# Optimization experiments

Measured on AMD Instinct MI355X. Metric: run time of the kernel, lower is better.

## Reference

```python
import jax, jax.numpy as jnp
import numpy as np

B, IN, H = 1024, 2048, 2048
W_BIT = A_BIT = I_BIT = R_BIT = 8


def fake_quant(x, bits):
    # brevitas CommonQuant: signed, narrow-range, const scale 1.0 ->
    # int scale s = 1/(2^(b-1)-1); q = clip(round(x/s), -n, n); dq = q*s.
    n = 2.0 ** (bits - 1) - 1.0
    q = jnp.clip(x * n, -n, n)
    q = q + jax.lax.stop_gradient(jnp.round(q) - q)  # STE round
    return q / n


def setup_inputs() -> dict:
    key = jax.random.key(0)
    ks = jax.random.split(key, 7)
    std = 1.0 / np.sqrt(H)  # reset_parameters: uniform(-std, std)
    return {
        "x": jax.random.normal(ks[0], (B, IN), jnp.float32),
        "hx": jax.random.normal(ks[1], (B, H), jnp.float32),
        "cx": jax.random.normal(ks[2], (B, H), jnp.float32),
        "w_x2h": jax.random.uniform(ks[3], (4 * H, IN), jnp.float32, -std, std),
        "b_x2h": jax.random.uniform(ks[4], (4 * H,), jnp.float32, -std, std),
        "w_h2h": jax.random.uniform(ks[5], (4 * H, H), jnp.float32, -std, std),
        "b_h2h": jax.random.uniform(ks[6], (4 * H,), jnp.float32, -std, std),
    }


def reference(x, hx, cx, w_x2h, b_x2h, w_h2h, b_h2h):
    x_q = fake_quant(x, I_BIT)                      # input_quant
    wx_q = fake_quant(w_x2h, W_BIT)                 # CommonWeightQuant
    wh_q = fake_quant(w_h2h, W_BIT)
    gates = (jnp.einsum('bi,gi->bg', x_q, wx_q) + b_x2h
             + jnp.einsum('bh,gh->bg', hx, wh_q) + b_h2h)  # [B, 4H]
    f, i, g, o = jnp.split(gates, 4, axis=1)        # forget, input, cell, out
    f = fake_quant(jax.nn.sigmoid(f), A_BIT)
    i = fake_quant(jax.nn.sigmoid(i), A_BIT)
    g = fake_quant(jnp.tanh(g), A_BIT)
    o = fake_quant(jax.nn.sigmoid(o), A_BIT)
    c_new = f * cx + i * g
    h_new = o * fake_quant(jnp.tanh(c_new), A_BIT)
    c_out = fake_quant(c_new, R_BIT)                # recurrent_quant
    return (h_new, c_out)
```

## Files before the change

kernel.cpp:

```cpp
#include <hip/hip_runtime.h>
#include <stdint.h>
#include <math.h>

typedef __attribute__((ext_vector_type(4))) int i32x4;
typedef __attribute__((ext_vector_type(4))) float f32x4;

#define GLD16(gp, lp)                                                     \
  __builtin_amdgcn_global_load_lds(                                       \
      (__attribute__((address_space(1))) void*)(gp),                      \
      (__attribute__((address_space(3))) void*)(lp), 16, 0, 0)

__global__ void __launch_bounds__(256) k_prep_w(const float* __restrict__ wx,
                                                const float* __restrict__ wh,
                                                signed char* __restrict__ Wq) {
  int i = blockIdx.x * 256 + threadIdx.x;
  int e = i << 2;
  int g = e >> 12;
  int c = e & 4095;
  const float* src = (c < 2048) ? (wx + g * 2048 + c) : (wh + g * 2048 + (c - 2048));
  float4 v = *(const float4*)src;
  char4 o;
  o.x = (signed char)(int)rint(fmin(fmax((double)v.x * 127.0, -127.0), 127.0));
  o.y = (signed char)(int)rint(fmin(fmax((double)v.y * 127.0, -127.0), 127.0));
  o.z = (signed char)(int)rint(fmin(fmax((double)v.z * 127.0, -127.0), 127.0));
  o.w = (signed char)(int)rint(fmin(fmax((double)v.w * 127.0, -127.0), 127.0));
  *(char4*)(Wq + e) = o;
}

__global__ void __launch_bounds__(256) k_prep_a(const float* __restrict__ x,
                                                const float* __restrict__ hx,
                                                signed char* __restrict__ Aq) {
  int i = blockIdx.x * 256 + threadIdx.x;
  int e = i << 2;
  int b = e >> 11;
  int c = e & 2047;
  float4 xv = *(const float4*)(x + b * 2048 + c);
  float4 hv = *(const float4*)(hx + b * 2048 + c);
  float xa[4] = {xv.x, xv.y, xv.z, xv.w};
  float ha[4] = {hv.x, hv.y, hv.z, hv.w};
  char4 q4, s1, s2, s3, s4, s5;
  signed char* qp = (signed char*)&q4;
  signed char* p1 = (signed char*)&s1;
  signed char* p2 = (signed char*)&s2;
  signed char* p3 = (signed char*)&s3;
  signed char* p4 = (signed char*)&s4;
  signed char* p5 = (signed char*)&s5;
  #pragma unroll
  for (int j = 0; j < 4; ++j) {
    qp[j] = (signed char)(int)rint(fmin(fmax((double)xa[j] * 127.0, -127.0), 127.0));
    double r = (double)ha[j];
    double d1 = rint(r * 16.0);     r -= d1 * 0x1p-4;
    double d2 = rint(r * 0x1p11);   r -= d2 * 0x1p-11;
    double d3 = rint(r * 0x1p18);   r -= d3 * 0x1p-18;
    double d4 = rint(r * 0x1p25);   r -= d4 * 0x1p-25;
    double d5 = rint(r * 0x1p32);
    p1[j] = (signed char)(int)d1;
    p2[j] = (signed char)(int)d2;
    p3[j] = (signed char)(int)d3;
    p4[j] = (signed char)(int)d4;
    p5[j] = (signed char)(int)d5;
  }
  size_t base = (size_t)b * 12288;
  *(char4*)(Aq + base + 0 * 2048 + c) = s5;
  *(char4*)(Aq + base + 1 * 2048 + c) = s4;
  *(char4*)(Aq + base + 2 * 2048 + c) = s3;
  *(char4*)(Aq + base + 3 * 2048 + c) = s2;
  *(char4*)(Aq + base + 4 * 2048 + c) = s1;
  *(char4*)(Aq + base + 5 * 2048 + c) = q4;
}

__global__ void __launch_bounds__(256, 3) k_gemm_lstm(
    const signed char* __restrict__ Aq, const signed char* __restrict__ Wq,
    const float* __restrict__ bx, const float* __restrict__ bh,
    const float* __restrict__ cx, float* __restrict__ out) {
  __shared__ __align__(16) signed char smem[24576];
  signed char* As = smem;
  signed char* Bs = smem + 16384;

  const int t  = threadIdx.x;
  const int wv = t >> 6;
  const int ln = t & 63;
  const int wm = wv & 1;
  const int wn = wv >> 1;
  const int lr = ln & 15;
  const int q  = ln >> 4;

  const int j0 = blockIdx.x * 16;
  const int m0 = blockIdx.y * 128;

  int sA[4];
  #pragma unroll
  for (int is = 0; is < 4; ++is) {
    int s = is * 256 + t;
    int r = s >> 3;
    int c = s & 7;
    int cp = c ^ (r & 7);
    sA[is] = (m0 + r) * 12288 + cp * 16;
  }
  int sB[2];
  #pragma unroll
  for (int is = 0; is < 2; ++is) {
    int s = is * 256 + t;
    int r = s >> 3;
    int c = s & 7;
    int cp = c ^ (r & 7);
    int wrow = (r >> 4) * 2048 + j0 + (r & 15);
    sB[is] = wrow * 4096 + cp * 16;
  }

  int aoff[4], boff[2];
  const int swz = lr & 7;
  #pragma unroll
  for (int mf = 0; mf < 4; ++mf)
    aoff[mf] = (wm * 64 + mf * 16 + lr) * 128 + ((q ^ swz) * 16);
  #pragma unroll
  for (int nf = 0; nf < 2; ++nf)
    boff[nf] = (wn * 32 + nf * 16 + lr) * 128 + ((q ^ swz) * 16);

  i32x4 acc[4][2];
  f32x4 Hh[4][2], Hl[4][2];
  #pragma unroll
  for (int mf = 0; mf < 4; ++mf)
    #pragma unroll
    for (int nf = 0; nf < 2; ++nf)
      acc[mf][nf] = (i32x4){0, 0, 0, 0};

  #pragma unroll 1
  for (int ph = 0; ph < 6; ++ph) {
    const int kA = ph * 2048;
    const int kB = (ph < 5) ? 2048 : 0;
    #pragma unroll 1
    for (int it = 0; it < 16; ++it) {
      const int kk = it * 128;
      __syncthreads();
      #pragma unroll
      for (int is = 0; is < 4; ++is)
        GLD16(Aq + sA[is] + kA + kk, As + is * 4096 + wv * 1024);
      #pragma unroll
      for (int is = 0; is < 2; ++is)
        GLD16(Wq + sB[is] + kB + kk, Bs + is * 4096 + wv * 1024);
      asm volatile("s_waitcnt vmcnt(0)" ::: "memory");
      __syncthreads();
      #pragma unroll
      for (int s = 0; s < 2; ++s) {
        const int sx = s << 6;
        i32x4 af[4], bf[2];
        #pragma unroll
        for (int mf = 0; mf < 4; ++mf) af[mf] = *(const i32x4*)&As[aoff[mf] ^ sx];
        #pragma unroll
        for (int nf = 0; nf < 2; ++nf) bf[nf] = *(const i32x4*)&Bs[boff[nf] ^ sx];
        #pragma unroll
        for (int mf = 0; mf < 4; ++mf)
          #pragma unroll
          for (int nf = 0; nf < 2; ++nf)
            acc[mf][nf] = __builtin_amdgcn_mfma_i32_16x16x64_i8(
                af[mf], bf[nf], acc[mf][nf], 0, 0, 0);
      }
    }
    if (ph == 0) {
      #pragma unroll
      for (int mf = 0; mf < 4; ++mf)
        #pragma unroll
        for (int nf = 0; nf < 2; ++nf) {
          #pragma unroll
          for (int r = 0; r < 4; ++r) {
            Hh[mf][nf][r] = (float)acc[mf][nf][r];
            Hl[mf][nf][r] = 0.f;
          }
          acc[mf][nf] = (i32x4){0, 0, 0, 0};
        }
    } else if (ph < 5) {
      #pragma unroll
      for (int mf = 0; mf < 4; ++mf)
        #pragma unroll
        for (int nf = 0; nf < 2; ++nf) {
          #pragma unroll
          for (int r = 0; r < 4; ++r) {
            float tv = Hh[mf][nf][r] * 0x1p-7f;
            float S  = (float)acc[mf][nf][r];
            float sm = tv + S;
            float z  = sm - tv;
            float e  = (tv - (sm - z)) + (S - z);
            Hl[mf][nf][r] = Hl[mf][nf][r] * 0x1p-7f + e;
            Hh[mf][nf][r] = sm;
          }
          acc[mf][nf] = (i32x4){0, 0, 0, 0};
        }
    }
  }

  const double invsq = 1.0 / 16129.0;
  const double hsc   = 0x1p-4 / 127.0;

  float (*Lgo)[128][17] = (float(*)[128][17])smem;

  __syncthreads();
  if (wn == 1) {
    #pragma unroll
    for (int mf = 0; mf < 4; ++mf) {
      #pragma unroll
      for (int nf = 0; nf < 2; ++nf) {
        int gate = 2 + nf;
        int gcol = gate * 2048 + j0 + lr;
        double bsum = (double)bx[gcol] + (double)bh[gcol];
        #pragma unroll
        for (int r = 0; r < 4; ++r) {
          double Sx = (double)acc[mf][nf][r];
          double Hd = ((double)Hh[mf][nf][r] + (double)Hl[mf][nf][r]) * hsc;
          double pre = Sx * invsq + Hd + bsum;
          double av = (gate == 2) ? tanh(pre) : (1.0 / (1.0 + exp(-pre)));
          double qv = rint(fmin(fmax(av * 127.0, -127.0), 127.0));
          int m = wm * 64 + mf * 16 + q * 4 + r;
          Lgo[nf][m][lr] = (float)qv;
        }
      }
    }
  }
  __syncthreads();
  if (wn == 0) {
    #pragma unroll
    for (int mf = 0; mf < 4; ++mf) {
      int gcf = j0 + lr;
      int gci = 2048 + j0 + lr;
      double bf_ = (double)bx[gcf] + (double)bh[gcf];
      double bi_ = (double)bx[gci] + (double)bh[gci];
      #pragma unroll
      for (int r = 0; r < 4; ++r) {
        int m = wm * 64 + mf * 16 + q * 4 + r;
        double fpre = (double)acc[mf][0][r] * invsq +
                      ((double)Hh[mf][0][r] + (double)Hl[mf][0][r]) * hsc + bf_;
        double ipre = (double)acc[mf][1][r] * invsq +
                      ((double)Hh[mf][1][r] + (double)Hl[mf][1][r]) * hsc + bi_;
        double fs = 1.0 / (1.0 + exp(-fpre));
        double is = 1.0 / (1.0 + exp(-ipre));
        double fv = rint(fmin(fmax(fs * 127.0, -127.0), 127.0)) / 127.0;
        double iv = rint(fmin(fmax(is * 127.0, -127.0), 127.0)) / 127.0;
        double gv = (double)Lgo[0][m][lr] / 127.0;
        double ov = (double)Lgo[1][m][lr] / 127.0;
        int row = m0 + m;
        int col = j0 + lr;
        double cn = fv * (double)cx[row * 2048 + col] + iv * gv;
        double tq = rint(fmin(fmax(tanh(cn) * 127.0, -127.0), 127.0)) / 127.0;
        double hv = ov * tq;
        double cq = rint(fmin(fmax(cn * 127.0, -127.0), 127.0)) / 127.0;
        out[row * 2048 + col] = (float)hv;
        out[2097152 + row * 2048 + col] = (float)cq;
      }
    }
  }
}

extern "C" void kernel_launch(void* const* d_in, const int* in_sizes, int n_in,
                              void* d_out, int out_size, void* d_ws, size_t ws_size,
                              hipStream_t stream) {
  const float* x  = (const float*)d_in[0];
  const float* hx = (const float*)d_in[1];
  const float* cx = (const float*)d_in[2];
  const float* wx = (const float*)d_in[3];
  const float* bx = (const float*)d_in[4];
  const float* wh = (const float*)d_in[5];
  const float* bh = (const float*)d_in[6];
  float* out = (float*)d_out;

  signed char* Wq = (signed char*)d_ws;
  signed char* Aq = (signed char*)d_ws + 33554432;

  k_prep_w<<<dim3(32768), dim3(256), 0, stream>>>(wx, wh, Wq);
  k_prep_a<<<dim3(2048), dim3(256), 0, stream>>>(x, hx, Aq);
  k_gemm_lstm<<<dim3(128, 8), dim3(256), 0, stream>>>(Aq, Wq, bx, bh, cx, out);
}
```

Baseline: 387.5 us.

## Widen GEMM tile to 32 columns, deepen K step, use float prep quantization

The prep kernels now quantize in float rather than double, cutting double-precision work. The GEMM block tile grows from 128x16 to 128x32 output columns per gate, with a 256-byte K step per iteration and a 64 KB LDS footprint. Occupancy drops to one block per CU, and the grid halves to 64x8. The hidden-state residue accumulation changes from a float two-sum to a plain double accumulator, trading register pressure and FP64 adds for simpler code.

```diff
diff --git a/kernel.cpp b/kernel.cpp
--- a/kernel.cpp
+++ b/kernel.cpp
@@ -3,7 +3,6 @@
 #include <math.h>
 
 typedef __attribute__((ext_vector_type(4))) int i32x4;
-typedef __attribute__((ext_vector_type(4))) float f32x4;
 
 #define GLD16(gp, lp)                                                     \
   __builtin_amdgcn_global_load_lds(                                       \
@@ -20,10 +19,10 @@
   const float* src = (c < 2048) ? (wx + g * 2048 + c) : (wh + g * 2048 + (c - 2048));
   float4 v = *(const float4*)src;
   char4 o;
-  o.x = (signed char)(int)rint(fmin(fmax((double)v.x * 127.0, -127.0), 127.0));
-  o.y = (signed char)(int)rint(fmin(fmax((double)v.y * 127.0, -127.0), 127.0));
-  o.z = (signed char)(int)rint(fmin(fmax((double)v.z * 127.0, -127.0), 127.0));
-  o.w = (signed char)(int)rint(fmin(fmax((double)v.w * 127.0, -127.0), 127.0));
+  o.x = (signed char)(int)rintf(fminf(fmaxf(v.x * 127.0f, -127.0f), 127.0f));
+  o.y = (signed char)(int)rintf(fminf(fmaxf(v.y * 127.0f, -127.0f), 127.0f));
+  o.z = (signed char)(int)rintf(fminf(fmaxf(v.z * 127.0f, -127.0f), 127.0f));
+  o.w = (signed char)(int)rintf(fminf(fmaxf(v.w * 127.0f, -127.0f), 127.0f));
   *(char4*)(Wq + e) = o;
 }
 
@@ -47,13 +46,13 @@
   signed char* p5 = (signed char*)&s5;
   #pragma unroll
   for (int j = 0; j < 4; ++j) {
-    qp[j] = (signed char)(int)rint(fmin(fmax((double)xa[j] * 127.0, -127.0), 127.0));
-    double r = (double)ha[j];
-    double d1 = rint(r * 16.0);     r -= d1 * 0x1p-4;
-    double d2 = rint(r * 0x1p11);   r -= d2 * 0x1p-11;
-    double d3 = rint(r * 0x1p18);   r -= d3 * 0x1p-18;
-    double d4 = rint(r * 0x1p25);   r -= d4 * 0x1p-25;
-    double d5 = rint(r * 0x1p32);
+    qp[j] = (signed char)(int)rintf(fminf(fmaxf(xa[j] * 127.0f, -127.0f), 127.0f));
+    float r = ha[j];
+    float d1 = rintf(r * 0x1p4f);    r -= d1 * 0x1p-4f;
+    float d2 = rintf(r * 0x1p11f);   r -= d2 * 0x1p-11f;
+    float d3 = rintf(r * 0x1p18f);   r -= d3 * 0x1p-18f;
+    float d4 = rintf(r * 0x1p25f);   r -= d4 * 0x1p-25f;
+    float d5 = rintf(r * 0x1p32f);
     p1[j] = (signed char)(int)d1;
     p2[j] = (signed char)(int)d2;
     p3[j] = (signed char)(int)d3;
@@ -69,13 +68,13 @@
   *(char4*)(Aq + base + 5 * 2048 + c) = q4;
 }
 
-__global__ void __launch_bounds__(256, 3) k_gemm_lstm(
+__global__ void __launch_bounds__(256, 1) k_gemm_lstm(
     const signed char* __restrict__ Aq, const signed char* __restrict__ Wq,
     const float* __restrict__ bx, const float* __restrict__ bh,
     const float* __restrict__ cx, float* __restrict__ out) {
-  __shared__ __align__(16) signed char smem[24576];
+  __shared__ __align__(16) signed char smem[65536];
   signed char* As = smem;
-  signed char* Bs = smem + 16384;
+  signed char* Bs = smem + 32768;
 
   const int t  = threadIdx.x;
   const int wv = t >> 6;
@@ -85,44 +84,35 @@
   const int lr = ln & 15;
   const int q  = ln >> 4;
 
-  const int j0 = blockIdx.x * 16;
+  const int j0 = blockIdx.x * 32;
   const int m0 = blockIdx.y * 128;
 
-  int sA[4];
-  #pragma unroll
-  for (int is = 0; is < 4; ++is) {
-    int s = is * 256 + t;
-    int r = s >> 3;
-    int c = s & 7;
-    int cp = c ^ (r & 7);
-    sA[is] = (m0 + r) * 12288 + cp * 16;
-  }
-  int sB[2];
-  #pragma unroll
-  for (int is = 0; is < 2; ++is) {
-    int s = is * 256 + t;
-    int r = s >> 3;
-    int c = s & 7;
-    int cp = c ^ (r & 7);
-    int wrow = (r >> 4) * 2048 + j0 + (r & 15);
-    sB[is] = wrow * 4096 + cp * 16;
-  }
-
-  int aoff[4], boff[2];
-  const int swz = lr & 7;
-  #pragma unroll
-  for (int mf = 0; mf < 4; ++mf)
-    aoff[mf] = (wm * 64 + mf * 16 + lr) * 128 + ((q ^ swz) * 16);
-  #pragma unroll
-  for (int nf = 0; nf < 2; ++nf)
-    boff[nf] = (wn * 32 + nf * 16 + lr) * 128 + ((q ^ swz) * 16);
-
-  i32x4 acc[4][2];
-  f32x4 Hh[4][2], Hl[4][2];
+  int sA[8], sB[8];
+  #pragma unroll
+  for (int i = 0; i < 8; ++i) {
+    int s = i * 256 + t;
+    int r = s >> 4;
+    int p = s & 15;
+    int c = p ^ (r & 15);
+    sA[i] = (m0 + r) * 12288 + c * 16;
+    int gate = r >> 5;
+    int jj = r & 31;
+    sB[i] = (gate * 2048 + j0 + jj) * 4096 + c * 16;
+  }
+
+  int aoff[4], boff[4];
+  #pragma unroll
+  for (int f = 0; f < 4; ++f) {
+    aoff[f] = (wm * 64 + f * 16 + lr) * 256;
+    boff[f] = 32768 + (wn * 64 + f * 16 + lr) * 256;
+  }
+
+  i32x4 acc[4][4];
+  double Hd[4][4][4];
   #pragma unroll
   for (int mf = 0; mf < 4; ++mf)
     #pragma unroll
-    for (int nf = 0; nf < 2; ++nf)
+    for (int nf = 0; nf < 4; ++nf)
       acc[mf][nf] = (i32x4){0, 0, 0, 0};
 
   #pragma unroll 1
@@ -130,88 +120,70 @@
     const int kA = ph * 2048;
     const int kB = (ph < 5) ? 2048 : 0;
     #pragma unroll 1
-    for (int it = 0; it < 16; ++it) {
-      const int kk = it * 128;
+    for (int it = 0; it < 8; ++it) {
+      const int kk = it * 256;
       __syncthreads();
       #pragma unroll
-      for (int is = 0; is < 4; ++is)
-        GLD16(Aq + sA[is] + kA + kk, As + is * 4096 + wv * 1024);
-      #pragma unroll
-      for (int is = 0; is < 2; ++is)
-        GLD16(Wq + sB[is] + kB + kk, Bs + is * 4096 + wv * 1024);
+      for (int i = 0; i < 8; ++i)
+        GLD16(Aq + sA[i] + kA + kk, As + i * 4096 + wv * 1024);
+      #pragma unroll
+      for (int i = 0; i < 8; ++i)
+        GLD16(Wq + sB[i] + kB + kk, Bs + i * 4096 + wv * 1024);
       asm volatile("s_waitcnt vmcnt(0)" ::: "memory");
       __syncthreads();
       #pragma unroll
-      for (int s = 0; s < 2; ++s) {
-        const int sx = s << 6;
-        i32x4 af[4], bf[2];
-        #pragma unroll
-        for (int mf = 0; mf < 4; ++mf) af[mf] = *(const i32x4*)&As[aoff[mf] ^ sx];
-        #pragma unroll
-        for (int nf = 0; nf < 2; ++nf) bf[nf] = *(const i32x4*)&Bs[boff[nf] ^ sx];
+      for (int kst = 0; kst < 4; ++kst) {
+        const int poff = ((kst * 4 + q) ^ lr) * 16;
+        i32x4 af[4], bf[4];
+        #pragma unroll
+        for (int mf = 0; mf < 4; ++mf) af[mf] = *(const i32x4*)&As[aoff[mf] + poff];
+        #pragma unroll
+        for (int nf = 0; nf < 4; ++nf) bf[nf] = *(const i32x4*)&smem[boff[nf] + poff];
         #pragma unroll
         for (int mf = 0; mf < 4; ++mf)
           #pragma unroll
-          for (int nf = 0; nf < 2; ++nf)
+          for (int nf = 0; nf < 4; ++nf)
             acc[mf][nf] = __builtin_amdgcn_mfma_i32_16x16x64_i8(
                 af[mf], bf[nf], acc[mf][nf], 0, 0, 0);
       }
     }
-    if (ph == 0) {
+    if (ph < 5) {
       #pragma unroll
       for (int mf = 0; mf < 4; ++mf)
         #pragma unroll
-        for (int nf = 0; nf < 2; ++nf) {
+        for (int nf = 0; nf < 4; ++nf) {
           #pragma unroll
           for (int r = 0; r < 4; ++r) {
-            Hh[mf][nf][r] = (float)acc[mf][nf][r];
-            Hl[mf][nf][r] = 0.f;
+            double S = (double)acc[mf][nf][r];
+            Hd[mf][nf][r] = (ph == 0) ? S : Hd[mf][nf][r] * 0x1p-7 + S;
           }
           acc[mf][nf] = (i32x4){0, 0, 0, 0};
         }
-    } else if (ph < 5) {
-      #pragma unroll
-      for (int mf = 0; mf < 4; ++mf)
-        #pragma unroll
-        for (int nf = 0; nf < 2; ++nf) {
-          #pragma unroll
-          for (int r = 0; r < 4; ++r) {
-            float tv = Hh[mf][nf][r] * 0x1p-7f;
-            float S  = (float)acc[mf][nf][r];
-            float sm = tv + S;
-            float z  = sm - tv;
-            float e  = (tv - (sm - z)) + (S - z);
-            Hl[mf][nf][r] = Hl[mf][nf][r] * 0x1p-7f + e;
-            Hh[mf][nf][r] = sm;
-          }
-          acc[mf][nf] = (i32x4){0, 0, 0, 0};
-        }
     }
   }
 
   const double invsq = 1.0 / 16129.0;
   const double hsc   = 0x1p-4 / 127.0;
 
-  float (*Lgo)[128][17] = (float(*)[128][17])smem;
+  float (*Lgo)[128][33] = (float(*)[128][33])smem;
 
   __syncthreads();
   if (wn == 1) {
     #pragma unroll
     for (int mf = 0; mf < 4; ++mf) {
       #pragma unroll
-      for (int nf = 0; nf < 2; ++nf) {
-        int gate = 2 + nf;
-        int gcol = gate * 2048 + j0 + lr;
+      for (int nf = 0; nf < 4; ++nf) {
+        int gate = 2 + (nf >> 1);
+        int jj = (nf & 1) * 16 + lr;
+        int gcol = gate * 2048 + j0 + jj;
         double bsum = (double)bx[gcol] + (double)bh[gcol];
         #pragma unroll
         for (int r = 0; r < 4; ++r) {
-          double Sx = (double)acc[mf][nf][r];
-          double Hd = ((double)Hh[mf][nf][r] + (double)Hl[mf][nf][r]) * hsc;
-          double pre = Sx * invsq + Hd + bsum;
+          double pre = (double)acc[mf][nf][r] * invsq + Hd[mf][nf][r] * hsc + bsum;
           double av = (gate == 2) ? tanh(pre) : (1.0 / (1.0 + exp(-pre)));
           double qv = rint(fmin(fmax(av * 127.0, -127.0), 127.0));
           int m = wm * 64 + mf * 16 + q * 4 + r;
-          Lgo[nf][m][lr] = (float)qv;
+          Lgo[gate - 2][m][jj] = (float)qv;
         }
       }
     }
@@ -220,31 +192,31 @@
   if (wn == 0) {
     #pragma unroll
     for (int mf = 0; mf < 4; ++mf) {
-      int gcf = j0 + lr;
-      int gci = 2048 + j0 + lr;
-      double bf_ = (double)bx[gcf] + (double)bh[gcf];
-      double bi_ = (double)bx[gci] + (double)bh[gci];
-      #pragma unroll
-      for (int r = 0; r < 4; ++r) {
-        int m = wm * 64 + mf * 16 + q * 4 + r;
-        double fpre = (double)acc[mf][0][r] * invsq +
-                      ((double)Hh[mf][0][r] + (double)Hl[mf][0][r]) * hsc + bf_;
-        double ipre = (double)acc[mf][1][r] * invsq +
-                      ((double)Hh[mf][1][r] + (double)Hl[mf][1][r]) * hsc + bi_;
-        double fs = 1.0 / (1.0 + exp(-fpre));
-        double is = 1.0 / (1.0 + exp(-ipre));
-        double fv = rint(fmin(fmax(fs * 127.0, -127.0), 127.0)) / 127.0;
-        double iv = rint(fmin(fmax(is * 127.0, -127.0), 127.0)) / 127.0;
-        double gv = (double)Lgo[0][m][lr] / 127.0;
-        double ov = (double)Lgo[1][m][lr] / 127.0;
-        int row = m0 + m;
-        int col = j0 + lr;
-        double cn = fv * (double)cx[row * 2048 + col] + iv * gv;
-        double tq = rint(fmin(fmax(tanh(cn) * 127.0, -127.0), 127.0)) / 127.0;
-        double hv = ov * tq;
-        double cq = rint(fmin(fmax(cn * 127.0, -127.0), 127.0)) / 127.0;
-        out[row * 2048 + col] = (float)hv;
-        out[2097152 + row * 2048 + col] = (float)cq;
+      #pragma unroll
+      for (int nfp = 0; nfp < 2; ++nfp) {
+        int jj = nfp * 16 + lr;
+        int gcf = j0 + jj;
+        int gci = 2048 + j0 + jj;
+        double bf_ = (double)bx[gcf] + (double)bh[gcf];
+        double bi_ = (double)bx[gci] + (double)bh[gci];
+        #pragma unroll
+        for (int r = 0; r < 4; ++r) {
+          int m = wm * 64 + mf * 16 + q * 4 + r;
+          double fpre = (double)acc[mf][nfp][r] * invsq + Hd[mf][nfp][r] * hsc + bf_;
+          double ipre = (double)acc[mf][nfp + 2][r] * invsq + Hd[mf][nfp + 2][r] * hsc + bi_;
+          double fv = rint(fmin(fmax((1.0 / (1.0 + exp(-fpre))) * 127.0, -127.0), 127.0)) / 127.0;
+          double iv = rint(fmin(fmax((1.0 / (1.0 + exp(-ipre))) * 127.0, -127.0), 127.0)) / 127.0;
+          double gv = (double)Lgo[0][m][jj] / 127.0;
+          double ov = (double)Lgo[1][m][jj] / 127.0;
+          int row = m0 + m;
+          int col = j0 + jj;
+          double cn = fv * (double)cx[row * 2048 + col] + iv * gv;
+          double tq = rint(fmin(fmax(tanh(cn) * 127.0, -127.0), 127.0)) / 127.0;
+          double hv = ov * tq;
+          double cq = rint(fmin(fmax(cn * 127.0, -127.0), 127.0)) / 127.0;
+          out[row * 2048 + col] = (float)hv;
+          out[2097152 + row * 2048 + col] = (float)cq;
+        }
       }
     }
   }
@@ -267,5 +239,5 @@
 
   k_prep_w<<<dim3(32768), dim3(256), 0, stream>>>(wx, wh, Wq);
   k_prep_a<<<dim3(2048), dim3(256), 0, stream>>>(x, hx, Aq);
-  k_gemm_lstm<<<dim3(128, 8), dim3(256), 0, stream>>>(Aq, Wq, bx, bh, cx, out);
-}
+  k_gemm_lstm<<<dim3(64, 8), dim3(256), 0, stream>>>(Aq, Wq, bx, bh, cx, out);
+}
```

After: 462.9 us. 19.5% more time.
